# Optimization experiments

Measured on AMD Instinct MI355X. Metric: run time of the kernel, lower is better.

The kernel has to match this reference:

```python
import jax, jax.numpy as jnp
import numpy as np

B, C, S, L = 16, 256, 64, 4096


def setup_inputs() -> dict:
    key = jax.random.key(0)
    k1, k2, k3 = jax.random.split(key, 3)
    x = jax.random.normal(k1, (B, C, L), dtype=jnp.float32)
    # parameters, matching the torch module's initialization
    log_dt = jax.random.uniform(k2, (C,), minval=-7.0, maxval=-3.0, dtype=jnp.float32)
    a_real = jnp.full((C, S), float(np.log(0.5)), dtype=jnp.float32)
    a_imag = jnp.tile((np.pi * jnp.arange(S, dtype=jnp.float32))[None, :], (C, 1))
    c = jax.random.normal(k3, (C, S, 2), dtype=jnp.float32)
    return {"x": x, "log_dt": log_dt, "a_real": a_real, "a_imag": a_imag, "c": c}


def _kernel(log_dt, a_real, a_imag, c, length):
    dt = jnp.exp(log_dt)                                   # [C]
    a = jax.lax.complex(-jnp.exp(a_real), a_imag)          # [C,S] complex64
    cc = jax.lax.complex(c[..., 0], c[..., 1])             # [C,S]
    a_dt = a * dt[:, None].astype(a.dtype)                 # [C,S]
    b_c = cc * (jnp.exp(a_dt) - 1.0) / a                   # [C,S]
    power = jnp.arange(length, dtype=jnp.float32)
    vander = jnp.exp(a_dt[..., None] * power)              # [C,S,L] complex64 Vandermonde
    return 2.0 * jnp.real(jnp.einsum('cs,csl->cl', b_c, vander))  # [C,L] float32


def reference(x, log_dt, a_real, a_imag, c):
    length = x.shape[-1]
    k = _kernel(log_dt, a_real, a_imag, c, length)         # [C,L]
    kf = jnp.fft.rfft(k, n=2 * length)                     # [C,L+1]
    xf = jnp.fft.rfft(x, n=2 * length)                     # [B,C,L+1]
    y = jnp.fft.irfft(kf * xf)[..., :length]               # [B,C,L]
    return y
```

## Files before the change

kernel.cpp:

```cpp
#include <hip/hip_runtime.h>

typedef __attribute__((ext_vector_type(8))) short bf16x8;
typedef __attribute__((ext_vector_type(4))) short short4v;
typedef __attribute__((ext_vector_type(4))) float f32x4;

#define NB 16
#define NC 256
#define NS 64
#define NL 4096
#define Q  64
#define NQ (NL / Q)

#define OFF_T   0
#define OFF_WR  8192
#define OFF_WI  16384
#define OFF_VR  24576
#define OFF_VM  32768
#define OFF_X   40960
#define OFF_HR  43008
#define OFF_HI  45056
#define OFF_PAR 47104
#define OFF_K   48128
#define OFF_KP  48384
#define LDS_SZ  49408

__device__ __forceinline__ int swz(int row, int bytecol) {
    return (row * 128 + bytecol) ^ ((row & 7) << 4);
}
__device__ __forceinline__ short f2bf(float f) {
    unsigned u = __builtin_bit_cast(unsigned, f);
    u = (u + 0x7FFFu + ((u >> 16) & 1u)) >> 16;
    return (short)u;
}

__global__ __launch_bounds__(256, 1) void s4d_mfma(const float* __restrict__ x,
                                                   const float* __restrict__ log_dt,
                                                   const float* __restrict__ a_real,
                                                   const float* __restrict__ a_imag,
                                                   const float* __restrict__ cv,
                                                   float* __restrict__ y) {
    __shared__ __align__(16) char lds[LDS_SZ];
    const int c = blockIdx.x;
    const int tid = threadIdx.x;
    const int l = tid & 63, w = tid >> 6;

    float* parF = (float*)(lds + OFF_PAR);
    float* kF   = (float*)(lds + OFF_K);
    float* kpF  = (float*)(lds + OFF_KP);

    if (tid < 64) {
        int s = tid;
        float dt = expf(log_dt[c]);
        float ar = -expf(a_real[c * 64 + s]);
        float ai = a_imag[c * 64 + s];
        float adr = ar * dt, adi = ai * dt;
        float e = expf(adr), sn, cs;
        sincosf(adi, &sn, &cs);
        float wr = e * cs, wi = e * sn;
        float inv = 1.0f / (ar * ar + ai * ai);
        float numr = wr - 1.0f, numi = wi;
        float qr = (numr * ar + numi * ai) * inv;
        float qi = (numi * ar - numr * ai) * inv;
        float c0 = cv[2 * (c * 64 + s)], c1 = cv[2 * (c * 64 + s) + 1];
        float br = c0 * qr - c1 * qi;
        float bi = c0 * qi + c1 * qr;
        parF[s] = adr; parF[64 + s] = adi;
        parF[128 + s] = 2.0f * br; parF[192 + s] = 2.0f * bi;
    }
    __syncthreads();

    {
        int d = tid & 63, part = tid >> 6;
        float ps = 0.0f;
        for (int s = part * 16; s < part * 16 + 16; ++s) {
            float e = expf(parF[s] * (float)d), sn, cs;
            sincosf(parF[64 + s] * (float)d, &sn, &cs);
            ps += e * (parF[128 + s] * cs - parF[192 + s] * sn);
        }
        kpF[part * 64 + d] = ps;
    }
    __syncthreads();
    if (tid < 64) kF[tid] = kpF[tid] + kpF[64 + tid] + kpF[128 + tid] + kpF[192 + tid];
    __syncthreads();

    {
        int t = tid >> 2, m0 = (tid & 3) * 16;
        for (int m = m0; m < m0 + 16; ++m) {
            float v = (t >= m) ? kF[t - m] : 0.0f;
            *(short*)(lds + OFF_T + swz(t, m * 2)) = f2bf(v);
        }
    }
    {
        int s = tid >> 2, m0 = (tid & 3) * 16;
        float adr = parF[s], adi = parF[64 + s];
        for (int m = m0; m < m0 + 16; ++m) {
            float p = (float)(63 - m);
            float e = expf(adr * p), sn, cs;
            sincosf(adi * p, &sn, &cs);
            *(short*)(lds + OFF_WR + swz(s, m * 2)) = f2bf(e * cs);
            *(short*)(lds + OFF_WI + swz(s, m * 2)) = f2bf(e * sn);
        }
    }
    {
        int t = tid >> 2, s0 = (tid & 3) * 16;
        float p = (float)(t + 1);
        for (int s = s0; s < s0 + 16; ++s) {
            float e = expf(parF[s] * p), sn, cs;
            sincosf(parF[64 + s] * p, &sn, &cs);
            float vr = e * (parF[128 + s] * cs - parF[192 + s] * sn);
            float vi = e * (parF[128 + s] * sn + parF[192 + s] * cs);
            *(short*)(lds + OFF_VR + swz(t, s * 2)) = f2bf(vr);
            *(short*)(lds + OFF_VM + swz(t, s * 2)) = f2bf(-vi);
        }
    }
    *(f32x4*)(lds + OFF_HR + tid * 16) = f32x4{0.f, 0.f, 0.f, 0.f};

    const float* xbase = x + ((size_t)(tid >> 4) * NC + c) * NL + (tid & 15) * 4;
    {
        float4 pf = *(const float4*)xbase;
        short4v xp = {f2bf(pf.x), f2bf(pf.y), f2bf(pf.z), f2bf(pf.w)};
        *(short4v*)(lds + OFF_X + swz(tid >> 4, (tid & 15) * 8)) = xp;
    }

    float wQr[4], wQi[4], Hr[4] = {0, 0, 0, 0}, Hi[4] = {0, 0, 0, 0};
#pragma unroll
    for (int j = 0; j < 4; ++j) {
        int s = 16 * w + (l >> 4) * 4 + j;
        float e = expf(64.0f * parF[s]), sn, cs;
        sincosf(64.0f * parF[64 + s], &sn, &cs);
        wQr[j] = e * cs; wQi[j] = e * sn;
    }
    __syncthreads();

    const int ar_ = l & 15;
    const int kb  = (l >> 4) * 16;
    const int rT = 16 * w + ar_;
    bf16x8 tA0 = *(const bf16x8*)(lds + OFF_T  + swz(rT, kb));
    bf16x8 tA1 = *(const bf16x8*)(lds + OFF_T  + swz(rT, kb + 64));
    bf16x8 wrA0 = *(const bf16x8*)(lds + OFF_WR + swz(rT, kb));
    bf16x8 wrA1 = *(const bf16x8*)(lds + OFF_WR + swz(rT, kb + 64));
    bf16x8 wiA0 = *(const bf16x8*)(lds + OFF_WI + swz(rT, kb));
    bf16x8 wiA1 = *(const bf16x8*)(lds + OFF_WI + swz(rT, kb + 64));
    bf16x8 vrA0 = *(const bf16x8*)(lds + OFF_VR + swz(rT, kb));
    bf16x8 vrA1 = *(const bf16x8*)(lds + OFF_VR + swz(rT, kb + 64));
    bf16x8 vmA0 = *(const bf16x8*)(lds + OFF_VM + swz(rT, kb));
    bf16x8 vmA1 = *(const bf16x8*)(lds + OFF_VM + swz(rT, kb + 64));

    const char* xB0  = lds + OFF_X  + swz(ar_, kb);
    const char* xB1  = lds + OFF_X  + swz(ar_, kb + 64);
    const char* hrB0 = lds + OFF_HR + swz(ar_, kb);
    const char* hrB1 = lds + OFF_HR + swz(ar_, kb + 64);
    const char* hiB0 = lds + OFF_HI + swz(ar_, kb);
    const char* hiB1 = lds + OFF_HI + swz(ar_, kb + 64);

    float* ybase = y + ((size_t)ar_ * NC + c) * NL + 16 * w + (l >> 4) * 4;

    for (int q = 0; q < NQ; ++q) {
        const int l0 = q * Q;
        float4 pf = *(const float4*)(xbase + ((q < NQ - 1) ? l0 + Q : 0));

        bf16x8 xb0 = *(const bf16x8*)xB0;
        bf16x8 xb1 = *(const bf16x8*)xB1;
        bf16x8 hr0 = *(const bf16x8*)hrB0;
        bf16x8 hr1 = *(const bf16x8*)hrB1;
        bf16x8 hi0 = *(const bf16x8*)hiB0;
        bf16x8 hi1 = *(const bf16x8*)hiB1;

        f32x4 yacc = {0.f, 0.f, 0.f, 0.f};
        f32x4 dr   = {0.f, 0.f, 0.f, 0.f};
        f32x4 di   = {0.f, 0.f, 0.f, 0.f};

        yacc = __builtin_amdgcn_mfma_f32_16x16x32_bf16(tA0, xb0, yacc, 0, 0, 0);
        yacc = __builtin_amdgcn_mfma_f32_16x16x32_bf16(tA1, xb1, yacc, 0, 0, 0);
        yacc = __builtin_amdgcn_mfma_f32_16x16x32_bf16(vrA0, hr0, yacc, 0, 0, 0);
        yacc = __builtin_amdgcn_mfma_f32_16x16x32_bf16(vrA1, hr1, yacc, 0, 0, 0);
        yacc = __builtin_amdgcn_mfma_f32_16x16x32_bf16(vmA0, hi0, yacc, 0, 0, 0);
        yacc = __builtin_amdgcn_mfma_f32_16x16x32_bf16(vmA1, hi1, yacc, 0, 0, 0);
        dr = __builtin_amdgcn_mfma_f32_16x16x32_bf16(wrA0, xb0, dr, 0, 0, 0);
        dr = __builtin_amdgcn_mfma_f32_16x16x32_bf16(wrA1, xb1, dr, 0, 0, 0);
        di = __builtin_amdgcn_mfma_f32_16x16x32_bf16(wiA0, xb0, di, 0, 0, 0);
        di = __builtin_amdgcn_mfma_f32_16x16x32_bf16(wiA1, xb1, di, 0, 0, 0);

#pragma unroll
        for (int j = 0; j < 4; ++j) {
            float nr = wQr[j] * Hr[j] - wQi[j] * Hi[j] + dr[j];
            float ni = wQr[j] * Hi[j] + wQi[j] * Hr[j] + di[j];
            Hr[j] = nr; Hi[j] = ni;
        }

        __syncthreads();

        short4v hrp = {f2bf(Hr[0]), f2bf(Hr[1]), f2bf(Hr[2]), f2bf(Hr[3])};
        short4v hip2 = {f2bf(Hi[0]), f2bf(Hi[1]), f2bf(Hi[2]), f2bf(Hi[3])};
        *(short4v*)(lds + OFF_HR + swz(ar_, 32 * w + (l >> 4) * 8)) = hrp;
        *(short4v*)(lds + OFF_HI + swz(ar_, 32 * w + (l >> 4) * 8)) = hip2;

        short4v xpn = {f2bf(pf.x), f2bf(pf.y), f2bf(pf.z), f2bf(pf.w)};
        *(short4v*)(lds + OFF_X + swz(tid >> 4, (tid & 15) * 8)) = xpn;

        *(f32x4*)(ybase + l0) = yacc;

        __syncthreads();
    }
}

extern "C" void kernel_launch(void* const* d_in, const int* in_sizes, int n_in,
                              void* d_out, int out_size, void* d_ws, size_t ws_size,
                              hipStream_t stream) {
    const float* x      = (const float*)d_in[0];
    const float* log_dt = (const float*)d_in[1];
    const float* a_real = (const float*)d_in[2];
    const float* a_imag = (const float*)d_in[3];
    const float* cv     = (const float*)d_in[4];
    float* yv = (float*)d_out;

    hipLaunchKernelGGL(s4d_mfma, dim3(NC), dim3(256), 0, stream,
                       x, log_dt, a_real, a_imag, cv, yv);
}
```

Baseline: 168.8 us.

## Split block into output and state-update wavegroups with deeper x prefetch

Doubles the block to 512 threads and gives each half its own role. Four waves compute the output MFMAs (Toeplitz plus state contribution), and the other four compute the chunk-state update MFMAs, do the recurrence, and load x into LDS. The x prefetch now runs two chunks ahead, the setup precompute is spread across the extra threads, and the output MFMA chain is split into three independent accumulators. This shortens the per-chunk serial dependency chain and overlaps the two roles, in exchange for more barrier participants and an LDS size change.

Measured after the change: 168.3 us. Within noise of the previous version (-0.3%).

```diff
diff --git a/kernel.cpp b/kernel.cpp
--- a/kernel.cpp
+++ b/kernel.cpp
@@ -22,7 +22,7 @@
 #define OFF_PAR 47104
 #define OFF_K   48128
 #define OFF_KP  48384
-#define LDS_SZ  49408
+#define LDS_SZ  50432
 
 __device__ __forceinline__ int swz(int row, int bytecol) {
     return (row * 128 + bytecol) ^ ((row & 7) << 4);
@@ -33,7 +33,7 @@
     return (short)u;
 }
 
-__global__ __launch_bounds__(256, 1) void s4d_mfma(const float* __restrict__ x,
+__global__ __launch_bounds__(512, 1) void s4d_mfma(const float* __restrict__ x,
                                                    const float* __restrict__ log_dt,
                                                    const float* __restrict__ a_real,
                                                    const float* __restrict__ a_imag,
@@ -43,6 +43,8 @@
     const int c = blockIdx.x;
     const int tid = threadIdx.x;
     const int l = tid & 63, w = tid >> 6;
+    const bool isY = (w < 4);
+    const int wl = w & 3;
 
     float* parF = (float*)(lds + OFF_PAR);
     float* kF   = (float*)(lds + OFF_K);
@@ -72,7 +74,7 @@
     {
         int d = tid & 63, part = tid >> 6;
         float ps = 0.0f;
-        for (int s = part * 16; s < part * 16 + 16; ++s) {
+        for (int s = part * 8; s < part * 8 + 8; ++s) {
             float e = expf(parF[s] * (float)d), sn, cs;
             sincosf(parF[64 + s] * (float)d, &sn, &cs);
             ps += e * (parF[128 + s] * cs - parF[192 + s] * sn);
@@ -80,20 +82,25 @@
         kpF[part * 64 + d] = ps;
     }
     __syncthreads();
-    if (tid < 64) kF[tid] = kpF[tid] + kpF[64 + tid] + kpF[128 + tid] + kpF[192 + tid];
-    __syncthreads();
-
-    {
-        int t = tid >> 2, m0 = (tid & 3) * 16;
-        for (int m = m0; m < m0 + 16; ++m) {
+    if (tid < 64) {
+        float a = 0.0f;
+#pragma unroll
+        for (int p = 0; p < 8; ++p) a += kpF[p * 64 + tid];
+        kF[tid] = a;
+    }
+    __syncthreads();
+
+    {
+        int t = tid >> 3, m0 = (tid & 7) * 8;
+        for (int m = m0; m < m0 + 8; ++m) {
             float v = (t >= m) ? kF[t - m] : 0.0f;
             *(short*)(lds + OFF_T + swz(t, m * 2)) = f2bf(v);
         }
     }
     {
-        int s = tid >> 2, m0 = (tid & 3) * 16;
+        int s = tid >> 3, m0 = (tid & 7) * 8;
         float adr = parF[s], adi = parF[64 + s];
-        for (int m = m0; m < m0 + 16; ++m) {
+        for (int m = m0; m < m0 + 8; ++m) {
             float p = (float)(63 - m);
             float e = expf(adr * p), sn, cs;
             sincosf(adi * p, &sn, &cs);
@@ -102,9 +109,9 @@
         }
     }
     {
-        int t = tid >> 2, s0 = (tid & 3) * 16;
+        int t = tid >> 3, s0 = (tid & 7) * 8;
         float p = (float)(t + 1);
-        for (int s = s0; s < s0 + 16; ++s) {
+        for (int s = s0; s < s0 + 8; ++s) {
             float e = expf(parF[s] * p), sn, cs;
             sincosf(parF[64 + s] * p, &sn, &cs);
             float vr = e * (parF[128 + s] * cs - parF[192 + s] * sn);
@@ -113,92 +120,109 @@
             *(short*)(lds + OFF_VM + swz(t, s * 2)) = f2bf(-vi);
         }
     }
-    *(f32x4*)(lds + OFF_HR + tid * 16) = f32x4{0.f, 0.f, 0.f, 0.f};
-
-    const float* xbase = x + ((size_t)(tid >> 4) * NC + c) * NL + (tid & 15) * 4;
-    {
-        float4 pf = *(const float4*)xbase;
-        short4v xp = {f2bf(pf.x), f2bf(pf.y), f2bf(pf.z), f2bf(pf.w)};
-        *(short4v*)(lds + OFF_X + swz(tid >> 4, (tid & 15) * 8)) = xp;
-    }
-
-    float wQr[4], wQi[4], Hr[4] = {0, 0, 0, 0}, Hi[4] = {0, 0, 0, 0};
-#pragma unroll
-    for (int j = 0; j < 4; ++j) {
-        int s = 16 * w + (l >> 4) * 4 + j;
-        float e = expf(64.0f * parF[s]), sn, cs;
-        sincosf(64.0f * parF[64 + s], &sn, &cs);
-        wQr[j] = e * cs; wQi[j] = e * sn;
-    }
-    __syncthreads();
+    if (tid < 256) {
+        *(f32x4*)(lds + OFF_HR + tid * 16) = f32x4{0.f, 0.f, 0.f, 0.f};
+    }
+
+    const int ltid = tid - 256;
+    const float* xbase = nullptr;
+    if (!isY) {
+        xbase = x + ((size_t)(ltid >> 4) * NC + c) * NL + (ltid & 15) * 4;
+        float4 p0 = *(const float4*)xbase;
+        short4v xp = {f2bf(p0.x), f2bf(p0.y), f2bf(p0.z), f2bf(p0.w)};
+        *(short4v*)(lds + OFF_X + swz(ltid >> 4, (ltid & 15) * 8)) = xp;
+    }
 
     const int ar_ = l & 15;
     const int kb  = (l >> 4) * 16;
-    const int rT = 16 * w + ar_;
-    bf16x8 tA0 = *(const bf16x8*)(lds + OFF_T  + swz(rT, kb));
-    bf16x8 tA1 = *(const bf16x8*)(lds + OFF_T  + swz(rT, kb + 64));
-    bf16x8 wrA0 = *(const bf16x8*)(lds + OFF_WR + swz(rT, kb));
-    bf16x8 wrA1 = *(const bf16x8*)(lds + OFF_WR + swz(rT, kb + 64));
-    bf16x8 wiA0 = *(const bf16x8*)(lds + OFF_WI + swz(rT, kb));
-    bf16x8 wiA1 = *(const bf16x8*)(lds + OFF_WI + swz(rT, kb + 64));
-    bf16x8 vrA0 = *(const bf16x8*)(lds + OFF_VR + swz(rT, kb));
-    bf16x8 vrA1 = *(const bf16x8*)(lds + OFF_VR + swz(rT, kb + 64));
-    bf16x8 vmA0 = *(const bf16x8*)(lds + OFF_VM + swz(rT, kb));
-    bf16x8 vmA1 = *(const bf16x8*)(lds + OFF_VM + swz(rT, kb + 64));
-
-    const char* xB0  = lds + OFF_X  + swz(ar_, kb);
-    const char* xB1  = lds + OFF_X  + swz(ar_, kb + 64);
-    const char* hrB0 = lds + OFF_HR + swz(ar_, kb);
-    const char* hrB1 = lds + OFF_HR + swz(ar_, kb + 64);
-    const char* hiB0 = lds + OFF_HI + swz(ar_, kb);
-    const char* hiB1 = lds + OFF_HI + swz(ar_, kb + 64);
-
-    float* ybase = y + ((size_t)ar_ * NC + c) * NL + 16 * w + (l >> 4) * 4;
-
-    for (int q = 0; q < NQ; ++q) {
-        const int l0 = q * Q;
-        float4 pf = *(const float4*)(xbase + ((q < NQ - 1) ? l0 + Q : 0));
-
-        bf16x8 xb0 = *(const bf16x8*)xB0;
-        bf16x8 xb1 = *(const bf16x8*)xB1;
-        bf16x8 hr0 = *(const bf16x8*)hrB0;
-        bf16x8 hr1 = *(const bf16x8*)hrB1;
-        bf16x8 hi0 = *(const bf16x8*)hiB0;
-        bf16x8 hi1 = *(const bf16x8*)hiB1;
-
-        f32x4 yacc = {0.f, 0.f, 0.f, 0.f};
-        f32x4 dr   = {0.f, 0.f, 0.f, 0.f};
-        f32x4 di   = {0.f, 0.f, 0.f, 0.f};
-
-        yacc = __builtin_amdgcn_mfma_f32_16x16x32_bf16(tA0, xb0, yacc, 0, 0, 0);
-        yacc = __builtin_amdgcn_mfma_f32_16x16x32_bf16(tA1, xb1, yacc, 0, 0, 0);
-        yacc = __builtin_amdgcn_mfma_f32_16x16x32_bf16(vrA0, hr0, yacc, 0, 0, 0);
-        yacc = __builtin_amdgcn_mfma_f32_16x16x32_bf16(vrA1, hr1, yacc, 0, 0, 0);
-        yacc = __builtin_amdgcn_mfma_f32_16x16x32_bf16(vmA0, hi0, yacc, 0, 0, 0);
-        yacc = __builtin_amdgcn_mfma_f32_16x16x32_bf16(vmA1, hi1, yacc, 0, 0, 0);
-        dr = __builtin_amdgcn_mfma_f32_16x16x32_bf16(wrA0, xb0, dr, 0, 0, 0);
-        dr = __builtin_amdgcn_mfma_f32_16x16x32_bf16(wrA1, xb1, dr, 0, 0, 0);
-        di = __builtin_amdgcn_mfma_f32_16x16x32_bf16(wiA0, xb0, di, 0, 0, 0);
-        di = __builtin_amdgcn_mfma_f32_16x16x32_bf16(wiA1, xb1, di, 0, 0, 0);
-
+    const int rT  = 16 * wl + ar_;
+
+    bf16x8 tA0, tA1, vrA0, vrA1, vmA0, vmA1;
+    bf16x8 wrA0, wrA1, wiA0, wiA1;
+    float wQr[4], wQi[4], Hr[4] = {0, 0, 0, 0}, Hi[4] = {0, 0, 0, 0};
+    float4 pfA = {0.f, 0.f, 0.f, 0.f};
+
+    if (!isY) {
 #pragma unroll
         for (int j = 0; j < 4; ++j) {
-            float nr = wQr[j] * Hr[j] - wQi[j] * Hi[j] + dr[j];
-            float ni = wQr[j] * Hi[j] + wQi[j] * Hr[j] + di[j];
-            Hr[j] = nr; Hi[j] = ni;
+            int s = 16 * wl + (l >> 4) * 4 + j;
+            float e = expf(64.0f * parF[s]), sn, cs;
+            sincosf(64.0f * parF[64 + s], &sn, &cs);
+            wQr[j] = e * cs; wQi[j] = e * sn;
+        }
+        pfA = *(const float4*)(xbase + Q);
+    }
+    __syncthreads();
+
+    if (isY) {
+        tA0  = *(const bf16x8*)(lds + OFF_T  + swz(rT, kb));
+        tA1  = *(const bf16x8*)(lds + OFF_T  + swz(rT, kb + 64));
+        vrA0 = *(const bf16x8*)(lds + OFF_VR + swz(rT, kb));
+        vrA1 = *(const bf16x8*)(lds + OFF_VR + swz(rT, kb + 64));
+        vmA0 = *(const bf16x8*)(lds + OFF_VM + swz(rT, kb));
+        vmA1 = *(const bf16x8*)(lds + OFF_VM + swz(rT, kb + 64));
+    } else {
+        wrA0 = *(const bf16x8*)(lds + OFF_WR + swz(rT, kb));
+        wrA1 = *(const bf16x8*)(lds + OFF_WR + swz(rT, kb + 64));
+        wiA0 = *(const bf16x8*)(lds + OFF_WI + swz(rT, kb));
+        wiA1 = *(const bf16x8*)(lds + OFF_WI + swz(rT, kb + 64));
+    }
+
+    float* ybase = y + ((size_t)ar_ * NC + c) * NL + 16 * wl + (l >> 4) * 4;
+
+    for (int q = 0; q < NQ; ++q) {
+        float4 pfB = {0.f, 0.f, 0.f, 0.f};
+        if (!isY)
+            pfB = *(const float4*)(xbase + ((q < NQ - 2) ? (q + 2) * Q : 0));
+
+        if (isY) {
+            bf16x8 xb0 = *(const bf16x8*)(lds + OFF_X  + swz(ar_, kb));
+            bf16x8 xb1 = *(const bf16x8*)(lds + OFF_X  + swz(ar_, kb + 64));
+            bf16x8 hr0 = *(const bf16x8*)(lds + OFF_HR + swz(ar_, kb));
+            bf16x8 hr1 = *(const bf16x8*)(lds + OFF_HR + swz(ar_, kb + 64));
+            bf16x8 hi0 = *(const bf16x8*)(lds + OFF_HI + swz(ar_, kb));
+            bf16x8 hi1 = *(const bf16x8*)(lds + OFF_HI + swz(ar_, kb + 64));
+            f32x4 aT = {0.f, 0.f, 0.f, 0.f};
+            f32x4 aR = {0.f, 0.f, 0.f, 0.f};
+            f32x4 aM = {0.f, 0.f, 0.f, 0.f};
+            aT = __builtin_amdgcn_mfma_f32_16x16x32_bf16(tA0,  xb0, aT, 0, 0, 0);
+            aR = __builtin_amdgcn_mfma_f32_16x16x32_bf16(vrA0, hr0, aR, 0, 0, 0);
+            aM = __builtin_amdgcn_mfma_f32_16x16x32_bf16(vmA0, hi0, aM, 0, 0, 0);
+            aT = __builtin_amdgcn_mfma_f32_16x16x32_bf16(tA1,  xb1, aT, 0, 0, 0);
+            aR = __builtin_amdgcn_mfma_f32_16x16x32_bf16(vrA1, hr1, aR, 0, 0, 0);
+            aM = __builtin_amdgcn_mfma_f32_16x16x32_bf16(vmA1, hi1, aM, 0, 0, 0);
+            f32x4 yacc = (aT + aR) + aM;
+            *(f32x4*)(ybase + q * Q) = yacc;
+        } else {
+            bf16x8 xb0 = *(const bf16x8*)(lds + OFF_X + swz(ar_, kb));
+            bf16x8 xb1 = *(const bf16x8*)(lds + OFF_X + swz(ar_, kb + 64));
+            f32x4 dr = {0.f, 0.f, 0.f, 0.f};
+            f32x4 di = {0.f, 0.f, 0.f, 0.f};
+            dr = __builtin_amdgcn_mfma_f32_16x16x32_bf16(wrA0, xb0, dr, 0, 0, 0);
+            di = __builtin_amdgcn_mfma_f32_16x16x32_bf16(wiA0, xb0, di, 0, 0, 0);
+            dr = __builtin_amdgcn_mfma_f32_16x16x32_bf16(wrA1, xb1, dr, 0, 0, 0);
+            di = __builtin_amdgcn_mfma_f32_16x16x32_bf16(wiA1, xb1, di, 0, 0, 0);
+#pragma unroll
+            for (int j = 0; j < 4; ++j) {
+                float nr = wQr[j] * Hr[j] - wQi[j] * Hi[j] + dr[j];
+                float ni = wQr[j] * Hi[j] + wQi[j] * Hr[j] + di[j];
+                Hr[j] = nr; Hi[j] = ni;
+            }
         }
 
         __syncthreads();
 
-        short4v hrp = {f2bf(Hr[0]), f2bf(Hr[1]), f2bf(Hr[2]), f2bf(Hr[3])};
-        short4v hip2 = {f2bf(Hi[0]), f2bf(Hi[1]), f2bf(Hi[2]), f2bf(Hi[3])};
-        *(short4v*)(lds + OFF_HR + swz(ar_, 32 * w + (l >> 4) * 8)) = hrp;
-        *(short4v*)(lds + OFF_HI + swz(ar_, 32 * w + (l >> 4) * 8)) = hip2;
-
-        short4v xpn = {f2bf(pf.x), f2bf(pf.y), f2bf(pf.z), f2bf(pf.w)};
-        *(short4v*)(lds + OFF_X + swz(tid >> 4, (tid & 15) * 8)) = xpn;
-
-        *(f32x4*)(ybase + l0) = yacc;
+        if (!isY) {
+            if (q < NQ - 1) {
+                short4v hrp = {f2bf(Hr[0]), f2bf(Hr[1]), f2bf(Hr[2]), f2bf(Hr[3])};
+                short4v hip2 = {f2bf(Hi[0]), f2bf(Hi[1]), f2bf(Hi[2]), f2bf(Hi[3])};
+                *(short4v*)(lds + OFF_HR + swz(ar_, 32 * wl + (l >> 4) * 8)) = hrp;
+                *(short4v*)(lds + OFF_HI + swz(ar_, 32 * wl + (l >> 4) * 8)) = hip2;
+                short4v xpn = {f2bf(pfA.x), f2bf(pfA.y), f2bf(pfA.z), f2bf(pfA.w)};
+                *(short4v*)(lds + OFF_X + swz(ltid >> 4, (ltid & 15) * 8)) = xpn;
+            }
+            pfA = pfB;
+        }
 
         __syncthreads();
     }
@@ -214,6 +238,6 @@
     const float* cv     = (const float*)d_in[4];
     float* yv = (float*)d_out;
 
-    hipLaunchKernelGGL(s4d_mfma, dim3(NC), dim3(256), 0, stream,
+    hipLaunchKernelGGL(s4d_mfma, dim3(NC), dim3(512), 0, stream,
                        x, log_dt, a_real, a_imag, cv, yv);
 }
```
